# Performance work log

Measured on AMD Instinct MI355X. Metric: run time of the kernel, lower is better.

The kernel has to match this reference:

```python
import jax, jax.numpy as jnp
import numpy as np


def setup_inputs() -> dict:
    key = jax.random.key(0)
    k1, k2, k3 = jax.random.split(key, 3)
    B, N, F, D = 8, 2048, 512, 512
    x = jax.random.normal(k1, (B, N, F), dtype=jnp.float32)
    a = jax.random.uniform(k2, (B, N, N), dtype=jnp.float32)
    kernel = jax.random.normal(k3, (F, D), dtype=jnp.float32) * (1.0 / np.sqrt(F))
    return {"x": x, "a": a, "kernel": kernel}


def reference(x, a, kernel):
    # t = a @ x : [B,N,N] x [B,N,F] -> [B,N,F]
    t = jnp.einsum('bnm,bmf->bnf', a, x)
    # feature transform: [B,N,F] x [F,D] -> [B,N,D]
    out = jnp.einsum('bnf,fd->bnd', t, kernel)
    # dropout is inference-mode (identity); no bias
    out = jax.nn.relu(out)
    # padded mask: zero rows of x produce zero outputs
    mask = (jnp.sum((x != 0).astype(jnp.float32), axis=-1, keepdims=True) > 0).astype(jnp.float32)
    return out * mask
```

## Files before the change

kernel.cpp:

```cpp
#include <hip/hip_runtime.h>

typedef __bf16 bf16x8 __attribute__((ext_vector_type(8)));
typedef float f32x4 __attribute__((ext_vector_type(4)));
typedef unsigned int u32x4 __attribute__((ext_vector_type(4)));

__device__ __forceinline__ unsigned short f2bf(float f) {
  unsigned u = __builtin_bit_cast(unsigned, f);
  u += 0x7FFFu + ((u >> 16) & 1u);
  return (unsigned short)(u >> 16);
}

__device__ __forceinline__ void gl2lds16(const void* g, void* l) {
  __builtin_amdgcn_global_load_lds((const __attribute__((address_space(1))) void*)g,
                                   (__attribute__((address_space(3))) void*)l, 16, 0, 0);
}

__device__ __forceinline__ bf16x8 gload16(const void* p) {
  bf16x8 r;
  asm volatile("global_load_dwordx4 %0, %1, off" : "=v"(r) : "v"(p));
  return r;
}

__device__ __forceinline__ bf16x8 cvt8v(f32x4 a, f32x4 b) {
  bf16x8 r;
  r[0] = (__bf16)a[0]; r[1] = (__bf16)a[1]; r[2] = (__bf16)a[2]; r[3] = (__bf16)a[3];
  r[4] = (__bf16)b[0]; r[5] = (__bf16)b[1]; r[6] = (__bf16)b[2]; r[7] = (__bf16)b[3];
  return r;
}

__global__ void transpose_cvt(const float* __restrict__ in, unsigned short* __restrict__ out) {
  __shared__ float tile[32][33];
  const int r0 = blockIdx.x * 32, c0 = blockIdx.y * 32;
  const int tx = threadIdx.x, ty = threadIdx.y;
#pragma unroll
  for (int i = 0; i < 4; ++i) tile[ty + i * 8][tx] = in[(size_t)(r0 + ty + i * 8) * 512 + c0 + tx];
  __syncthreads();
#pragma unroll
  for (int i = 0; i < 4; ++i) {
    const int cc = ty + i * 8;
    out[(size_t)(c0 + cc) * 512 + r0 + tx] = f2bf(tile[tx][cc]);
  }
}

template <int APITCH, int BPITCH, int NT, bool IS_Y>
__global__ __launch_bounds__(512, 1) void gemm_pipe(const float* __restrict__ A0,
                                                    const unsigned short* __restrict__ B0,
                                                    unsigned short* __restrict__ yT,
                                                    int* __restrict__ mask,
                                                    float* __restrict__ out) {
  __shared__ __align__(16) float Abuf[4][64 * 64];

  const int bid = blockIdx.x;
  int b, m0loc;
  const float* Ab;
  const unsigned short* Bb;
  if constexpr (IS_Y) {
    b = bid >> 5;
    m0loc = (bid & 31) * 64;
    Ab = A0 + (size_t)bid * 64 * APITCH;
    Bb = B0;
  } else {
    b = bid & 7;
    m0loc = (bid >> 3) * 64;
    Ab = A0 + ((size_t)b * 2048 + m0loc) * APITCH;
    Bb = B0 + (size_t)b * 512 * 2048;
  }

  const int tid = threadIdx.x, lane = tid & 63, w = tid >> 6;
  const int r = lane & 15, hi = lane >> 4;

  const int p16 = lane & 15;
  const int srow0 = w * 8 + (lane >> 4);
  const float* gs0 = Ab + (size_t)srow0 * APITCH + ((p16 ^ (srow0 & 7)) * 4);
  const float* gs1 = Ab + (size_t)(srow0 + 4) * APITCH + ((p16 ^ ((srow0 + 4) & 7)) * 4);
  char* lbase = (char*)&Abuf[0][0] + w * 2048;

  const unsigned short* bp[4];
#pragma unroll
  for (int ni = 0; ni < 4; ++ni)
    bp[ni] = Bb + (size_t)(w * 64 + ni * 16 + r) * BPITCH + hi * 8;

  int aoff[4][2][2];
#pragma unroll
  for (int mi = 0; mi < 4; ++mi)
#pragma unroll
    for (int kk = 0; kk < 2; ++kk) {
      const int row = mi * 16 + r;
      const int c0 = kk * 8 + hi * 2;
#pragma unroll
      for (int h = 0; h < 2; ++h)
        aoff[mi][kk][h] = row * 256 + (((c0 + h) ^ (r & 7)) << 4);
    }

  f32x4 acc[4][4] = {};
  unsigned anz[4] = {0u, 0u, 0u, 0u};
  bf16x8 bc[4][2], bn[4][2];

#pragma unroll
  for (int ni = 0; ni < 4; ++ni)
#pragma unroll
    for (int kk = 0; kk < 2; ++kk) bc[ni][kk] = gload16(bp[ni] + kk * 32);
  __builtin_amdgcn_sched_barrier(0);
#pragma unroll
  for (int s = 0; s < 3; ++s) {
    gl2lds16(gs0 + s * 64, lbase + s * 16384);
    gl2lds16(gs1 + s * 64, lbase + s * 16384 + 1024);
  }
  __builtin_amdgcn_sched_barrier(0);

#define PIPE_BODY(T, BCC, BCN)                                                    \
  {                                                                               \
    asm volatile("s_waitcnt vmcnt(2)");                                           \
    __builtin_amdgcn_sched_barrier(0);                                            \
    __builtin_amdgcn_s_barrier();                                                 \
    const int tb1 = ((T) + 1 < NT) ? (T) + 1 : NT - 1;                            \
    const int ta3 = ((T) + 3 < NT) ? (T) + 3 : NT - 1;                            \
    const int slot = ((T) + 3) & 3;                                               \
    _Pragma("unroll") for (int ni = 0; ni < 4; ++ni)                              \
        _Pragma("unroll") for (int kk = 0; kk < 2; ++kk)                          \
            BCN[ni][kk] = gload16(bp[ni] + tb1 * 64 + kk * 32);                   \
    __builtin_amdgcn_sched_barrier(0);                                            \
    gl2lds16(gs0 + ta3 * 64, lbase + slot * 16384);                               \
    gl2lds16(gs1 + ta3 * 64, lbase + slot * 16384 + 1024);                        \
    __builtin_amdgcn_sched_barrier(0);                                            \
    const char* sb = (const char*)&Abuf[(T) & 3][0];                              \
    _Pragma("unroll") for (int mi = 0; mi < 4; ++mi)                              \
        _Pragma("unroll") for (int kk = 0; kk < 2; ++kk) {                        \
          f32x4 lo = *(const f32x4*)(sb + aoff[mi][kk][0]);                       \
          f32x4 hh = *(const f32x4*)(sb + aoff[mi][kk][1]);                       \
          if constexpr (IS_Y) {                                                   \
            if (w == 0) {                                                         \
              u32x4 u0 = __builtin_bit_cast(u32x4, lo);                           \
              u32x4 u1 = __builtin_bit_cast(u32x4, hh);                           \
              anz[mi] |= (u0[0] | u0[1] | u0[2] | u0[3] | u1[0] | u1[1] | u1[2] | \
                          u1[3]) & 0x7fffffffu;                                   \
            }                                                                     \
          }                                                                       \
          bf16x8 af = cvt8v(lo, hh);                                              \
          _Pragma("unroll") for (int ni = 0; ni < 4; ++ni)                        \
              acc[mi][ni] = __builtin_amdgcn_mfma_f32_16x16x32_bf16(              \
                  af, BCC[ni][kk], acc[mi][ni], 0, 0, 0);                         \
        }                                                                         \
  }

#pragma unroll 1
  for (int t = 0; t < NT; t += 2) {
    PIPE_BODY(t, bc, bn)
    PIPE_BODY(t + 1, bn, bc)
  }
#undef PIPE_BODY

  asm volatile("s_waitcnt vmcnt(0)");

  if constexpr (IS_Y) {
    if (w == 0) {
#pragma unroll
      for (int mi = 0; mi < 4; ++mi) {
        unsigned v = anz[mi];
        v |= __shfl_xor(v, 16);
        v |= __shfl_xor(v, 32);
        if (hi == 0) mask[b * 2048 + m0loc + mi * 16 + r] = (v != 0u) ? 1 : 0;
      }
    }
#pragma unroll
    for (int mi = 0; mi < 4; ++mi)
#pragma unroll
      for (int ni = 0; ni < 4; ++ni) {
        const int col = w * 64 + ni * 16 + r;
        ushort4 s;
        s.x = f2bf(acc[mi][ni][0]);
        s.y = f2bf(acc[mi][ni][1]);
        s.z = f2bf(acc[mi][ni][2]);
        s.w = f2bf(acc[mi][ni][3]);
        *(ushort4*)(yT + (((size_t)b * 512 + col) << 11) + m0loc + mi * 16 + hi * 4) = s;
      }
  } else {
    const int* mrow = mask + b * 2048 + m0loc;
#pragma unroll
    for (int mi = 0; mi < 4; ++mi) {
      const int4 mv = *(const int4*)(mrow + mi * 16 + hi * 4);
      const int mvv[4] = {mv.x, mv.y, mv.z, mv.w};
#pragma unroll
      for (int ni = 0; ni < 4; ++ni) {
        const int col = w * 64 + ni * 16 + r;
        float* op = out + ((size_t)(b * 2048 + m0loc + mi * 16 + hi * 4)) * 512 + col;
#pragma unroll
        for (int rr = 0; rr < 4; ++rr) {
          float v = fmaxf(acc[mi][ni][rr], 0.0f);
          if (mvv[rr] == 0) v = 0.0f;
          op[(size_t)rr * 512] = v;
        }
      }
    }
  }
}

extern "C" void kernel_launch(void* const* d_in, const int* in_sizes, int n_in,
                              void* d_out, int out_size, void* d_ws, size_t ws_size,
                              hipStream_t stream) {
  const float* x = (const float*)d_in[0];
  const float* a = (const float*)d_in[1];
  const float* wk = (const float*)d_in[2];
  float* out = (float*)d_out;

  char* ws = (char*)d_ws;
  unsigned short* wT = (unsigned short*)ws;
  unsigned short* yT = (unsigned short*)(ws + (1u << 19));
  int* mask = (int*)(ws + (1u << 19) + (16u << 20));

  transpose_cvt<<<dim3(16, 16), dim3(32, 8), 0, stream>>>(wk, wT);
  gemm_pipe<512, 512, 8, true><<<256, 512, 0, stream>>>(x, wT, yT, mask, nullptr);
  gemm_pipe<2048, 2048, 32, false><<<256, 512, 0, stream>>>(a, yT, nullptr, mask, out);
}
```

Before: 113.3 us.

## Switch GEMMs to 128x128 tiles with LDS-staged A/B fragments, 2 blocks/CU

Both GEMM kernels are rebuilt around 128x128 output tiles computed by 4 waves, each owning a 64x64 sub-tile. Both A and B are staged into LDS through global_load_lds in a fragment-ordered layout, replacing the direct B register loads and the swizzled A buffer. The launch changes from 256 blocks of 512 threads at occupancy 1 to 512 blocks of 256 threads at occupancy 2. This raises reuse of each loaded A and B element, but it drops the 4-stage prefetch pipeline in favour of a single buffer with two __syncthreads per k-step, so load latency is no longer overlapped within a block.

```diff
diff --git a/kernel.cpp b/kernel.cpp
--- a/kernel.cpp
+++ b/kernel.cpp
@@ -13,12 +13,6 @@
 __device__ __forceinline__ void gl2lds16(const void* g, void* l) {
   __builtin_amdgcn_global_load_lds((const __attribute__((address_space(1))) void*)g,
                                    (__attribute__((address_space(3))) void*)l, 16, 0, 0);
-}
-
-__device__ __forceinline__ bf16x8 gload16(const void* p) {
-  bf16x8 r;
-  asm volatile("global_load_dwordx4 %0, %1, off" : "=v"(r) : "v"(p));
-  return r;
 }
 
 __device__ __forceinline__ bf16x8 cvt8v(f32x4 a, f32x4 b) {
@@ -43,147 +37,126 @@
 }
 
 template <int APITCH, int BPITCH, int NT, bool IS_Y>
-__global__ __launch_bounds__(512, 1) void gemm_pipe(const float* __restrict__ A0,
+__global__ __launch_bounds__(256, 2) void gemm_frag(const float* __restrict__ A0,
                                                     const unsigned short* __restrict__ B0,
                                                     unsigned short* __restrict__ yT,
                                                     int* __restrict__ mask,
                                                     float* __restrict__ out) {
-  __shared__ __align__(16) float Abuf[4][64 * 64];
+  __shared__ __align__(16) char lds[49152];
+  char* ldsA = lds;
+  char* ldsB = lds + 32768;
 
   const int bid = blockIdx.x;
-  int b, m0loc;
+  int b, m0loc, n0;
   const float* Ab;
   const unsigned short* Bb;
   if constexpr (IS_Y) {
-    b = bid >> 5;
-    m0loc = (bid & 31) * 64;
-    Ab = A0 + (size_t)bid * 64 * APITCH;
-    Bb = B0;
+    const int mt = bid >> 2, nt = bid & 3;
+    b = mt >> 4;
+    m0loc = (mt & 15) * 128;
+    n0 = nt * 128;
+    Ab = A0 + ((size_t)b * 2048 + m0loc) * APITCH;
+    Bb = B0 + (size_t)n0 * BPITCH;
   } else {
     b = bid & 7;
-    m0loc = (bid >> 3) * 64;
+    const int idx = bid >> 3;
+    m0loc = (idx & 15) * 128;
+    n0 = (idx >> 4) * 128;
     Ab = A0 + ((size_t)b * 2048 + m0loc) * APITCH;
-    Bb = B0 + (size_t)b * 512 * 2048;
+    Bb = B0 + ((size_t)b * 512 + n0) * BPITCH;
   }
 
-  const int tid = threadIdx.x, lane = tid & 63, w = tid >> 6;
-  const int r = lane & 15, hi = lane >> 4;
+  const int tid = threadIdx.x, w = tid >> 6, lane = tid & 63;
+  const int wr = w >> 1, wc = w & 1, r = lane & 15, hi = lane >> 4;
+  const int lof = lane * 16;
 
-  const int p16 = lane & 15;
-  const int srow0 = w * 8 + (lane >> 4);
-  const float* gs0 = Ab + (size_t)srow0 * APITCH + ((p16 ^ (srow0 & 7)) * 4);
-  const float* gs1 = Ab + (size_t)(srow0 + 4) * APITCH + ((p16 ^ ((srow0 + 4) & 7)) * 4);
-  char* lbase = (char*)&Abuf[0][0] + w * 2048;
-
-  const unsigned short* bp[4];
-#pragma unroll
-  for (int ni = 0; ni < 4; ++ni)
-    bp[ni] = Bb + (size_t)(w * 64 + ni * 16 + r) * BPITCH + hi * 8;
-
-  int aoff[4][2][2];
-#pragma unroll
-  for (int mi = 0; mi < 4; ++mi)
-#pragma unroll
-    for (int kk = 0; kk < 2; ++kk) {
-      const int row = mi * 16 + r;
-      const int c0 = kk * 8 + hi * 2;
-#pragma unroll
-      for (int h = 0; h < 2; ++h)
-        aoff[mi][kk][h] = row * 256 + (((c0 + h) ^ (r & 7)) << 4);
-    }
+  const float* apv = Ab + (size_t)(lane & 15) * APITCH + (lane >> 4) * 8;
+  const unsigned short* bpv = Bb + (size_t)(lane & 15) * BPITCH + (lane >> 4) * 8;
 
   f32x4 acc[4][4] = {};
   unsigned anz[4] = {0u, 0u, 0u, 0u};
-  bf16x8 bc[4][2], bn[4][2];
+
+#pragma unroll 1
+  for (int t = 0; t < NT; ++t) {
+    const int k0 = t * 64;
+#pragma unroll
+    for (int j = 0; j < 8; ++j) {
+      const int g = w * 8 + j;
+      const int gwr = g >> 4, gmi = (g >> 2) & 3, gkk = (g >> 1) & 1, gh = g & 1;
+      gl2lds16(apv + k0 + (size_t)(gwr * 64 + gmi * 16) * APITCH + gkk * 32 + gh * 4,
+               ldsA + g * 1024);
+    }
+#pragma unroll
+    for (int j = 0; j < 4; ++j) {
+      const int g2 = w * 4 + j;
+      const int gwc = g2 >> 3, gni = (g2 >> 1) & 3, gkk = g2 & 1;
+      gl2lds16(bpv + k0 + (size_t)(gwc * 64 + gni * 16) * BPITCH + gkk * 32,
+               ldsB + g2 * 1024);
+    }
+    __syncthreads();
+
+    bf16x8 bf[4][2];
+#pragma unroll
+    for (int ni = 0; ni < 4; ++ni)
+#pragma unroll
+      for (int kk = 0; kk < 2; ++kk)
+        bf[ni][kk] = *(const bf16x8*)(ldsB + (((wc << 3) | (ni << 1) | kk) << 10) + lof);
 
 #pragma unroll
-  for (int ni = 0; ni < 4; ++ni)
+    for (int kk = 0; kk < 2; ++kk)
 #pragma unroll
-    for (int kk = 0; kk < 2; ++kk) bc[ni][kk] = gload16(bp[ni] + kk * 32);
-  __builtin_amdgcn_sched_barrier(0);
+      for (int mi = 0; mi < 4; ++mi) {
+        f32x4 lo = *(const f32x4*)(ldsA + (((wr << 4) | (mi << 2) | (kk << 1)) << 10) + lof);
+        f32x4 hh = *(const f32x4*)(ldsA + ((((wr << 4) | (mi << 2) | (kk << 1)) | 1) << 10) + lof);
+        if constexpr (IS_Y) {
+          if (wc == 0) {
+            u32x4 u0 = __builtin_bit_cast(u32x4, lo), u1 = __builtin_bit_cast(u32x4, hh);
+            anz[mi] |= (u0[0] | u0[1] | u0[2] | u0[3] | u1[0] | u1[1] | u1[2] | u1[3]) &
+                       0x7fffffffu;
+          }
+        }
+        bf16x8 af = cvt8v(lo, hh);
 #pragma unroll
-  for (int s = 0; s < 3; ++s) {
-    gl2lds16(gs0 + s * 64, lbase + s * 16384);
-    gl2lds16(gs1 + s * 64, lbase + s * 16384 + 1024);
-  }
-  __builtin_amdgcn_sched_barrier(0);
-
-#define PIPE_BODY(T, BCC, BCN)                                                    \
-  {                                                                               \
-    asm volatile("s_waitcnt vmcnt(2)");                                           \
-    __builtin_amdgcn_sched_barrier(0);                                            \
-    __builtin_amdgcn_s_barrier();                                                 \
-    const int tb1 = ((T) + 1 < NT) ? (T) + 1 : NT - 1;                            \
-    const int ta3 = ((T) + 3 < NT) ? (T) + 3 : NT - 1;                            \
-    const int slot = ((T) + 3) & 3;                                               \
-    _Pragma("unroll") for (int ni = 0; ni < 4; ++ni)                              \
-        _Pragma("unroll") for (int kk = 0; kk < 2; ++kk)                          \
-            BCN[ni][kk] = gload16(bp[ni] + tb1 * 64 + kk * 32);                   \
-    __builtin_amdgcn_sched_barrier(0);                                            \
-    gl2lds16(gs0 + ta3 * 64, lbase + slot * 16384);                               \
-    gl2lds16(gs1 + ta3 * 64, lbase + slot * 16384 + 1024);                        \
-    __builtin_amdgcn_sched_barrier(0);                                            \
-    const char* sb = (const char*)&Abuf[(T) & 3][0];                              \
-    _Pragma("unroll") for (int mi = 0; mi < 4; ++mi)                              \
-        _Pragma("unroll") for (int kk = 0; kk < 2; ++kk) {                        \
-          f32x4 lo = *(const f32x4*)(sb + aoff[mi][kk][0]);                       \
-          f32x4 hh = *(const f32x4*)(sb + aoff[mi][kk][1]);                       \
-          if constexpr (IS_Y) {                                                   \
-            if (w == 0) {                                                         \
-              u32x4 u0 = __builtin_bit_cast(u32x4, lo);                           \
-              u32x4 u1 = __builtin_bit_cast(u32x4, hh);                           \
-              anz[mi] |= (u0[0] | u0[1] | u0[2] | u0[3] | u1[0] | u1[1] | u1[2] | \
-                          u1[3]) & 0x7fffffffu;                                   \
-            }                                                                     \
-          }                                                                       \
-          bf16x8 af = cvt8v(lo, hh);                                              \
-          _Pragma("unroll") for (int ni = 0; ni < 4; ++ni)                        \
-              acc[mi][ni] = __builtin_amdgcn_mfma_f32_16x16x32_bf16(              \
-                  af, BCC[ni][kk], acc[mi][ni], 0, 0, 0);                         \
-        }                                                                         \
+        for (int ni = 0; ni < 4; ++ni)
+          acc[mi][ni] =
+              __builtin_amdgcn_mfma_f32_16x16x32_bf16(af, bf[ni][kk], acc[mi][ni], 0, 0, 0);
+      }
+    if (t + 1 < NT) __syncthreads();
   }
 
-#pragma unroll 1
-  for (int t = 0; t < NT; t += 2) {
-    PIPE_BODY(t, bc, bn)
-    PIPE_BODY(t + 1, bn, bc)
-  }
-#undef PIPE_BODY
-
-  asm volatile("s_waitcnt vmcnt(0)");
-
   if constexpr (IS_Y) {
-    if (w == 0) {
+    if (wc == 0) {
 #pragma unroll
       for (int mi = 0; mi < 4; ++mi) {
         unsigned v = anz[mi];
         v |= __shfl_xor(v, 16);
         v |= __shfl_xor(v, 32);
-        if (hi == 0) mask[b * 2048 + m0loc + mi * 16 + r] = (v != 0u) ? 1 : 0;
+        if (hi == 0) mask[b * 2048 + m0loc + wr * 64 + mi * 16 + r] = (v != 0u) ? 1 : 0;
       }
     }
 #pragma unroll
     for (int mi = 0; mi < 4; ++mi)
 #pragma unroll
       for (int ni = 0; ni < 4; ++ni) {
-        const int col = w * 64 + ni * 16 + r;
+        const int col = n0 + wc * 64 + ni * 16 + r;
+        const int nrow = m0loc + wr * 64 + mi * 16 + hi * 4;
         ushort4 s;
         s.x = f2bf(acc[mi][ni][0]);
         s.y = f2bf(acc[mi][ni][1]);
         s.z = f2bf(acc[mi][ni][2]);
         s.w = f2bf(acc[mi][ni][3]);
-        *(ushort4*)(yT + (((size_t)b * 512 + col) << 11) + m0loc + mi * 16 + hi * 4) = s;
+        *(ushort4*)(yT + (((size_t)b * 512 + col) << 11) + nrow) = s;
       }
   } else {
-    const int* mrow = mask + b * 2048 + m0loc;
+    const int* mrow = mask + b * 2048 + m0loc + wr * 64;
 #pragma unroll
     for (int mi = 0; mi < 4; ++mi) {
       const int4 mv = *(const int4*)(mrow + mi * 16 + hi * 4);
       const int mvv[4] = {mv.x, mv.y, mv.z, mv.w};
 #pragma unroll
       for (int ni = 0; ni < 4; ++ni) {
-        const int col = w * 64 + ni * 16 + r;
-        float* op = out + ((size_t)(b * 2048 + m0loc + mi * 16 + hi * 4)) * 512 + col;
+        const int col = n0 + wc * 64 + ni * 16 + r;
+        float* op = out + (size_t)(b * 2048 + m0loc + wr * 64 + mi * 16 + hi * 4) * 512 + col;
 #pragma unroll
         for (int rr = 0; rr < 4; ++rr) {
           float v = fmaxf(acc[mi][ni][rr], 0.0f);
@@ -209,6 +182,6 @@
   int* mask = (int*)(ws + (1u << 19) + (16u << 20));
 
   transpose_cvt<<<dim3(16, 16), dim3(32, 8), 0, stream>>>(wk, wT);
-  gemm_pipe<512, 512, 8, true><<<256, 512, 0, stream>>>(x, wT, yT, mask, nullptr);
-  gemm_pipe<2048, 2048, 32, false><<<256, 512, 0, stream>>>(a, yT, nullptr, mask, out);
+  gemm_frag<512, 512, 8, true><<<512, 256, 0, stream>>>(x, wT, yT, mask, nullptr);
+  gemm_frag<2048, 2048, 32, false><<<512, 256, 0, stream>>>(a, yT, nullptr, mask, out);
 }
```

Result: slower. 130.4 us (+15.1%).
